# Optimization experiments

Measured on AMD Instinct MI355X. Metric: run time of the kernel, lower is better.

The kernel has to match this reference:

```python
import jax, jax.numpy as jnp
import numpy as np

T, B, N_LABELS = 128, 512, 512
HIDDEN, SEMANTIC = 1024, 1024
THRESHOLD, DECAY = 1.0, 0.95


def setup_inputs() -> dict:
    key = jax.random.key(0)
    k1, k2, k3 = jax.random.split(key, 3)
    spike_seq = (jax.random.uniform(k1, (T, B, N_LABELS)) < 0.1).astype(jnp.float32)
    W1 = jax.random.normal(k2, (HIDDEN, N_LABELS), dtype=jnp.float32) * 0.05
    W2 = jax.random.normal(k3, (SEMANTIC, HIDDEN), dtype=jnp.float32) * 0.05
    return {"spike_seq": spike_seq, "W1": W1, "W2": W2}


def reference(spike_seq, W1, W2):
    """LIF two-layer SNN. LIF step: v = decay*v + input; spike = (v > threshold);
    hard reset to zero on spike. Returns time-averaged spikes of layer1 and layer2."""
    dtype = spike_seq.dtype
    Bsz = spike_seq.shape[1]

    def lif(v, x):
        v = DECAY * v + x
        spk = (v > THRESHOLD).astype(dtype)
        return spk, v * (1.0 - spk)

    def step(carry, x_t):
        v1, v2 = carry
        spk1, v1 = lif(v1, x_t @ W1.T)          # (B, HIDDEN)
        spk2, v2 = lif(v2, spk1 @ W2.T)         # (B, SEMANTIC)
        return (v1, v2), (spk1, spk2)

    v1_0 = jnp.zeros((Bsz, W1.shape[0]), dtype)
    v2_0 = jnp.zeros((Bsz, W2.shape[0]), dtype)
    _, (spk1_all, spk2_all) = jax.lax.scan(step, (v1_0, v2_0), spike_seq)
    return spk1_all.mean(axis=0), spk2_all.mean(axis=0)
```

## Files before the change

kernel.cpp:

```cpp
#include <hip/hip_runtime.h>


#define T_STEPS 128
#define BATCH   512
#define NLAB    512
#define HID     1024
#define SEM     1024

__global__ __launch_bounds__(256) void transpose32(const float* __restrict__ in,
                                                   float* __restrict__ out,
                                                   int R, int C) {
    __shared__ float tile[32][33];
    const int c0 = blockIdx.x * 32, r0 = blockIdx.y * 32;
    const int x = threadIdx.x, y0 = threadIdx.y;
#pragma unroll
    for (int i = 0; i < 32; i += 8)
        tile[y0 + i][x] = in[(size_t)(r0 + y0 + i) * C + (c0 + x)];
    __syncthreads();
#pragma unroll
    for (int i = 0; i < 32; i += 8)
        out[(size_t)(c0 + y0 + i) * R + (r0 + x)] = tile[x][y0 + i];
}

__device__ __forceinline__ void gather4(const int* __restrict__ list,
                                        int lo, int hi,
                                        const float* __restrict__ base,
                                        float s[4]) {
    float s0 = 0.0f, s1 = 0.0f, s2 = 0.0f, s3 = 0.0f;
    int k = lo;
    for (; k + 16 <= hi; k += 16) {
        float4 wv[16];
#pragma unroll
        for (int j = 0; j < 16; ++j) {
            const int row = __builtin_amdgcn_readfirstlane(list[k + j]);
            wv[j] = *reinterpret_cast<const float4*>(base + ((size_t)row << 10));
        }
#pragma unroll
        for (int j = 0; j < 16; ++j) {
            s0 = __fadd_rn(s0, wv[j].x);
            s1 = __fadd_rn(s1, wv[j].y);
            s2 = __fadd_rn(s2, wv[j].z);
            s3 = __fadd_rn(s3, wv[j].w);
        }
    }
    for (; k + 8 <= hi; k += 8) {
        float4 wv[8];
#pragma unroll
        for (int j = 0; j < 8; ++j) {
            const int row = __builtin_amdgcn_readfirstlane(list[k + j]);
            wv[j] = *reinterpret_cast<const float4*>(base + ((size_t)row << 10));
        }
#pragma unroll
        for (int j = 0; j < 8; ++j) {
            s0 = __fadd_rn(s0, wv[j].x);
            s1 = __fadd_rn(s1, wv[j].y);
            s2 = __fadd_rn(s2, wv[j].z);
            s3 = __fadd_rn(s3, wv[j].w);
        }
    }
    for (; k < hi; ++k) {
        const int row = __builtin_amdgcn_readfirstlane(list[k]);
        const float4 wv = *reinterpret_cast<const float4*>(base + ((size_t)row << 10));
        s0 = __fadd_rn(s0, wv.x);
        s1 = __fadd_rn(s1, wv.y);
        s2 = __fadd_rn(s2, wv.z);
        s3 = __fadd_rn(s3, wv.w);
    }
    s[0] = s0; s[1] = s1; s[2] = s2; s[3] = s3;
}

__global__ __launch_bounds__(256)
void snn_kernel(const float* __restrict__ spikes,
                const float* __restrict__ w1t,
                const float* __restrict__ w2t,
                float* __restrict__ out) {
    __shared__ int wc1[4];
    __shared__ int wc1p;
    __shared__ int wc2[4];
    __shared__ int wc2p[3];
    __shared__ __align__(16) int list1[NLAB];
    __shared__ __align__(16) int list2[HID];

    const int b    = blockIdx.x;
    const int tid  = threadIdx.x;
    const int w    = tid >> 6;
    const int lane = tid & 63;
    const unsigned long long below = (1ull << lane) - 1ull;

    float v1[4] = {0.0f, 0.0f, 0.0f, 0.0f};
    float v2[4] = {0.0f, 0.0f, 0.0f, 0.0f};
    int   c1[4] = {0, 0, 0, 0};
    int   c2[4] = {0, 0, 0, 0};

    const float* sp_b = spikes + (size_t)b * NLAB + 2 * tid;
    const float* w1b  = w1t + 4 * tid;
    const float* w2b  = w2t + 4 * tid;

    float2 sv = *reinterpret_cast<const float2*>(sp_b);

    for (int t = 0; t < T_STEPS; ++t) {
        const bool a0 = (sv.x != 0.0f);
        const bool a1 = (sv.y != 0.0f);
        const unsigned long long m0 = __ballot(a0);
        const unsigned long long m1 = __ballot(a1);
        if (lane == 0) {
            wc1[w] = __popcll(m0) + __popcll(m1);
            if (w == 2)
                wc1p = __popcll(m0 & 0xFFFFFFFFull) + __popcll(m1 & 0xFFFFFFFFull);
        }
        const int pre1 = __popcll(m0 & below) + __popcll(m1 & below);
        __syncthreads();

        {
            int base = 0;
            for (int i = 0; i < w; ++i) base += wc1[i];
            int p = base + pre1;
            if (a0) list1[p++] = 2 * tid;
            if (a1) list1[p]   = 2 * tid + 1;
        }
        __syncthreads();

        if (t + 1 < T_STEPS)
            sv = *reinterpret_cast<const float2*>(sp_b + (size_t)(t + 1) * (BATCH * NLAB));

        bool spk0, spk1, spk2, spk3;
        int  preh;
        {
            const int nA = wc1[0] + wc1[1] + wc1p;
            const int n1 = wc1[0] + wc1[1] + wc1[2] + wc1[3];
            float xA[4], xB[4];
            gather4(list1, 0,  nA, w1b, xA);
            gather4(list1, nA, n1, w1b, xB);
#pragma unroll
            for (int j = 0; j < 4; ++j) {
                const float x1 = __fadd_rn(xA[j], xB[j]);
                v1[j] = __fadd_rn(__fmul_rn(0.95f, v1[j]), x1);
            }
            spk0 = (v1[0] > 1.0f); if (spk0) { c1[0]++; v1[0] = 0.0f; }
            spk1 = (v1[1] > 1.0f); if (spk1) { c1[1]++; v1[1] = 0.0f; }
            spk2 = (v1[2] > 1.0f); if (spk2) { c1[2]++; v1[2] = 0.0f; }
            spk3 = (v1[3] > 1.0f); if (spk3) { c1[3]++; v1[3] = 0.0f; }

            const unsigned long long b0 = __ballot(spk0);
            const unsigned long long b1 = __ballot(spk1);
            const unsigned long long b2 = __ballot(spk2);
            const unsigned long long b3 = __ballot(spk3);
            if (lane == 0) {
                wc2[w] = __popcll(b0) + __popcll(b1) + __popcll(b2) + __popcll(b3);
                if (w == 1)
                    wc2p[0] = __popcll(b0 & 0xFFFFull) + __popcll(b1 & 0xFFFFull)
                            + __popcll(b2 & 0xFFFFull) + __popcll(b3 & 0xFFFFull);
                if (w == 2)
                    wc2p[1] = __popcll(b0 & 0xFFFFFFFFull) + __popcll(b1 & 0xFFFFFFFFull)
                            + __popcll(b2 & 0xFFFFFFFFull) + __popcll(b3 & 0xFFFFFFFFull);
                if (w == 3)
                    wc2p[2] = __popcll(b0 & 0xFFFFFFFFFFFFull) + __popcll(b1 & 0xFFFFFFFFFFFFull)
                            + __popcll(b2 & 0xFFFFFFFFFFFFull) + __popcll(b3 & 0xFFFFFFFFFFFFull);
            }
            preh = __popcll(b0 & below) + __popcll(b1 & below)
                 + __popcll(b2 & below) + __popcll(b3 & below);
        }
        __syncthreads();

        {
            int base = 0;
            for (int i = 0; i < w; ++i) base += wc2[i];
            int p = base + preh;
            if (spk0) list2[p++] = 4 * tid;
            if (spk1) list2[p++] = 4 * tid + 1;
            if (spk2) list2[p++] = 4 * tid + 2;
            if (spk3) list2[p]   = 4 * tid + 3;
        }
        __syncthreads();

        {
            const int nA = wc2[0] + wc2p[0];
            const int nB = wc2[0] + wc2[1] + wc2p[1];
            const int nC = wc2[0] + wc2[1] + wc2[2] + wc2p[2];
            const int n2 = wc2[0] + wc2[1] + wc2[2] + wc2[3];
            float t1[4], t2[4], t3[4], t4[4];
            gather4(list2, 0,  nA, w2b, t1);
            gather4(list2, nA, nB, w2b, t2);
            gather4(list2, nB, nC, w2b, t3);
            gather4(list2, nC, n2, w2b, t4);
#pragma unroll
            for (int j = 0; j < 4; ++j) {
                const float x2 = __fadd_rn(__fadd_rn(__fadd_rn(t1[j], t2[j]), t3[j]), t4[j]);
                v2[j] = __fadd_rn(__fmul_rn(0.95f, v2[j]), x2);
                if (v2[j] > 1.0f) { c2[j]++; v2[j] = 0.0f; }
            }
        }
        __syncthreads();
    }

    const float sc = 1.0f / 128.0f;
    const float4 o1 = make_float4((float)c1[0] * sc, (float)c1[1] * sc,
                                  (float)c1[2] * sc, (float)c1[3] * sc);
    *reinterpret_cast<float4*>(out + (size_t)b * HID + 4 * tid) = o1;
    const float4 o2 = make_float4((float)c2[0] * sc, (float)c2[1] * sc,
                                  (float)c2[2] * sc, (float)c2[3] * sc);
    *reinterpret_cast<float4*>(out + (size_t)BATCH * HID + (size_t)b * SEM + 4 * tid) = o2;
}

extern "C" void kernel_launch(void* const* d_in, const int* in_sizes, int n_in,
                              void* d_out, int out_size, void* d_ws, size_t ws_size,
                              hipStream_t stream) {
    const float* spikes = (const float*)d_in[0];
    const float* W1     = (const float*)d_in[1];
    const float* W2     = (const float*)d_in[2];
    float* out = (float*)d_out;

    float* w1t = (float*)d_ws;
    float* w2t = w1t + (size_t)NLAB * HID;

    dim3 tb(32, 8);
    transpose32<<<dim3(NLAB / 32, HID / 32), tb, 0, stream>>>(W1, w1t, HID, NLAB);
    transpose32<<<dim3(HID / 32, SEM / 32),  tb, 0, stream>>>(W2, w2t, SEM, HID);

    snn_kernel<<<BATCH, 256, 0, stream>>>(spikes, w1t, w2t, out);
}
```

Before: 1.563 ms.

## Process two batch rows per block sharing union spike lists and weight loads

Each block now handles two batch rows. It builds one union list of active inputs and hidden spikes, with per-row mask bits packed into each entry, so each gathered weight row is loaded once and applied to both rows through masked packed FMAs. This cuts weight gather traffic per row and halves the grid to 256 blocks, which may underfill the GPU's CUs. The union lists are longer than either row's own list, and the masked FMA arithmetic (adding 0*w instead of skipping) could differ slightly from the original sequential adds.

```diff
diff --git a/kernel.cpp b/kernel.cpp
--- a/kernel.cpp
+++ b/kernel.cpp
@@ -6,6 +6,8 @@
 #define NLAB    512
 #define HID     1024
 #define SEM     1024
+
+typedef float f32x2 __attribute__((ext_vector_type(2)));
 
 __global__ __launch_bounds__(256) void transpose32(const float* __restrict__ in,
                                                    float* __restrict__ out,
@@ -22,51 +24,66 @@
         out[(size_t)(c0 + y0 + i) * R + (r0 + x)] = tile[x][y0 + i];
 }
 
-__device__ __forceinline__ void gather4(const int* __restrict__ list,
+__device__ __forceinline__ void gatherU(const int* __restrict__ list,
                                         int lo, int hi,
                                         const float* __restrict__ base,
-                                        float s[4]) {
-    float s0 = 0.0f, s1 = 0.0f, s2 = 0.0f, s3 = 0.0f;
+                                        f32x2 s[4]) {
+    f32x2 s00 = {0.0f, 0.0f}, s01 = {0.0f, 0.0f};
+    f32x2 s10 = {0.0f, 0.0f}, s11 = {0.0f, 0.0f};
     int k = lo;
     for (; k + 16 <= hi; k += 16) {
+        int    e[16];
         float4 wv[16];
 #pragma unroll
         for (int j = 0; j < 16; ++j) {
-            const int row = __builtin_amdgcn_readfirstlane(list[k + j]);
-            wv[j] = *reinterpret_cast<const float4*>(base + ((size_t)row << 10));
+            e[j] = __builtin_amdgcn_readfirstlane(list[k + j]);
+            wv[j] = *reinterpret_cast<const float4*>(base + ((size_t)(e[j] & 0xFFFF) << 10));
         }
 #pragma unroll
         for (int j = 0; j < 16; ++j) {
-            s0 = __fadd_rn(s0, wv[j].x);
-            s1 = __fadd_rn(s1, wv[j].y);
-            s2 = __fadd_rn(s2, wv[j].z);
-            s3 = __fadd_rn(s3, wv[j].w);
+            const float f0 = (e[j] & 0x10000) ? 1.0f : 0.0f;
+            const float f1 = (e[j] & 0x20000) ? 1.0f : 0.0f;
+            const f32x2 m0 = {f0, f0}, m1 = {f1, f1};
+            const f32x2 w01 = {wv[j].x, wv[j].y}, w23 = {wv[j].z, wv[j].w};
+            s00 = __builtin_elementwise_fma(m0, w01, s00);
+            s01 = __builtin_elementwise_fma(m0, w23, s01);
+            s10 = __builtin_elementwise_fma(m1, w01, s10);
+            s11 = __builtin_elementwise_fma(m1, w23, s11);
         }
     }
     for (; k + 8 <= hi; k += 8) {
+        int    e[8];
         float4 wv[8];
 #pragma unroll
         for (int j = 0; j < 8; ++j) {
-            const int row = __builtin_amdgcn_readfirstlane(list[k + j]);
-            wv[j] = *reinterpret_cast<const float4*>(base + ((size_t)row << 10));
+            e[j] = __builtin_amdgcn_readfirstlane(list[k + j]);
+            wv[j] = *reinterpret_cast<const float4*>(base + ((size_t)(e[j] & 0xFFFF) << 10));
         }
 #pragma unroll
         for (int j = 0; j < 8; ++j) {
-            s0 = __fadd_rn(s0, wv[j].x);
-            s1 = __fadd_rn(s1, wv[j].y);
-            s2 = __fadd_rn(s2, wv[j].z);
-            s3 = __fadd_rn(s3, wv[j].w);
+            const float f0 = (e[j] & 0x10000) ? 1.0f : 0.0f;
+            const float f1 = (e[j] & 0x20000) ? 1.0f : 0.0f;
+            const f32x2 m0 = {f0, f0}, m1 = {f1, f1};
+            const f32x2 w01 = {wv[j].x, wv[j].y}, w23 = {wv[j].z, wv[j].w};
+            s00 = __builtin_elementwise_fma(m0, w01, s00);
+            s01 = __builtin_elementwise_fma(m0, w23, s01);
+            s10 = __builtin_elementwise_fma(m1, w01, s10);
+            s11 = __builtin_elementwise_fma(m1, w23, s11);
         }
     }
     for (; k < hi; ++k) {
-        const int row = __builtin_amdgcn_readfirstlane(list[k]);
-        const float4 wv = *reinterpret_cast<const float4*>(base + ((size_t)row << 10));
-        s0 = __fadd_rn(s0, wv.x);
-        s1 = __fadd_rn(s1, wv.y);
-        s2 = __fadd_rn(s2, wv.z);
-        s3 = __fadd_rn(s3, wv.w);
-    }
-    s[0] = s0; s[1] = s1; s[2] = s2; s[3] = s3;
+        const int e = __builtin_amdgcn_readfirstlane(list[k]);
+        const float4 wv = *reinterpret_cast<const float4*>(base + ((size_t)(e & 0xFFFF) << 10));
+        const float f0 = (e & 0x10000) ? 1.0f : 0.0f;
+        const float f1 = (e & 0x20000) ? 1.0f : 0.0f;
+        const f32x2 m0 = {f0, f0}, m1 = {f1, f1};
+        const f32x2 w01 = {wv.x, wv.y}, w23 = {wv.z, wv.w};
+        s00 = __builtin_elementwise_fma(m0, w01, s00);
+        s01 = __builtin_elementwise_fma(m0, w23, s01);
+        s10 = __builtin_elementwise_fma(m1, w01, s10);
+        s11 = __builtin_elementwise_fma(m1, w23, s11);
+    }
+    s[0] = s00; s[1] = s01; s[2] = s10; s[3] = s11;
 }
 
 __global__ __launch_bounds__(256)
@@ -81,28 +98,33 @@
     __shared__ __align__(16) int list1[NLAB];
     __shared__ __align__(16) int list2[HID];
 
-    const int b    = blockIdx.x;
     const int tid  = threadIdx.x;
     const int w    = tid >> 6;
     const int lane = tid & 63;
     const unsigned long long below = (1ull << lane) - 1ull;
 
-    float v1[4] = {0.0f, 0.0f, 0.0f, 0.0f};
-    float v2[4] = {0.0f, 0.0f, 0.0f, 0.0f};
-    int   c1[4] = {0, 0, 0, 0};
-    int   c2[4] = {0, 0, 0, 0};
-
-    const float* sp_b = spikes + (size_t)b * NLAB + 2 * tid;
-    const float* w1b  = w1t + 4 * tid;
-    const float* w2b  = w2t + 4 * tid;
-
-    float2 sv = *reinterpret_cast<const float2*>(sp_b);
+    const int b0 = 2 * blockIdx.x;
+
+    f32x2 v1[4] = {{0,0},{0,0},{0,0},{0,0}};
+    f32x2 v2[4] = {{0,0},{0,0},{0,0},{0,0}};
+    int   c1[8] = {0,0,0,0,0,0,0,0};
+    int   c2[8] = {0,0,0,0,0,0,0,0};
+
+    const float* sp0 = spikes + (size_t)b0 * NLAB + 2 * tid;
+    const float* sp1 = sp0 + NLAB;
+    const float* w1b = w1t + 4 * tid;
+    const float* w2b = w2t + 4 * tid;
+
+    float2 sv0 = *reinterpret_cast<const float2*>(sp0);
+    float2 sv1 = *reinterpret_cast<const float2*>(sp1);
 
     for (int t = 0; t < T_STEPS; ++t) {
-        const bool a0 = (sv.x != 0.0f);
-        const bool a1 = (sv.y != 0.0f);
-        const unsigned long long m0 = __ballot(a0);
-        const unsigned long long m1 = __ballot(a1);
+        const bool a00 = (sv0.x != 0.0f), a01 = (sv0.y != 0.0f);
+        const bool a10 = (sv1.x != 0.0f), a11 = (sv1.y != 0.0f);
+        const bool u0 = a00 | a10;
+        const bool u1 = a01 | a11;
+        const unsigned long long m0 = __ballot(u0);
+        const unsigned long long m1 = __ballot(u1);
         if (lane == 0) {
             wc1[w] = __popcll(m0) + __popcll(m1);
             if (w == 2)
@@ -115,50 +137,60 @@
             int base = 0;
             for (int i = 0; i < w; ++i) base += wc1[i];
             int p = base + pre1;
-            if (a0) list1[p++] = 2 * tid;
-            if (a1) list1[p]   = 2 * tid + 1;
-        }
-        __syncthreads();
-
-        if (t + 1 < T_STEPS)
-            sv = *reinterpret_cast<const float2*>(sp_b + (size_t)(t + 1) * (BATCH * NLAB));
-
-        bool spk0, spk1, spk2, spk3;
+            if (u0) list1[p++] = (2 * tid)     | (a00 ? 0x10000 : 0) | (a10 ? 0x20000 : 0);
+            if (u1) list1[p]   = (2 * tid + 1) | (a01 ? 0x10000 : 0) | (a11 ? 0x20000 : 0);
+        }
+        __syncthreads();
+
+        if (t + 1 < T_STEPS) {
+            sv0 = *reinterpret_cast<const float2*>(sp0 + (size_t)(t + 1) * (BATCH * NLAB));
+            sv1 = *reinterpret_cast<const float2*>(sp1 + (size_t)(t + 1) * (BATCH * NLAB));
+        }
+
+        bool sp00, sp01, sp02, sp03, sp10, sp11, sp12, sp13;
         int  preh;
         {
             const int nA = wc1[0] + wc1[1] + wc1p;
             const int n1 = wc1[0] + wc1[1] + wc1[2] + wc1[3];
-            float xA[4], xB[4];
-            gather4(list1, 0,  nA, w1b, xA);
-            gather4(list1, nA, n1, w1b, xB);
+            f32x2 xA[4], xB[4];
+            gatherU(list1, 0,  nA, w1b, xA);
+            gatherU(list1, nA, n1, w1b, xB);
 #pragma unroll
             for (int j = 0; j < 4; ++j) {
-                const float x1 = __fadd_rn(xA[j], xB[j]);
-                v1[j] = __fadd_rn(__fmul_rn(0.95f, v1[j]), x1);
+                const f32x2 x1 = xA[j] + xB[j];
+                v1[j] = (v1[j] * 0.95f) + x1;
             }
-            spk0 = (v1[0] > 1.0f); if (spk0) { c1[0]++; v1[0] = 0.0f; }
-            spk1 = (v1[1] > 1.0f); if (spk1) { c1[1]++; v1[1] = 0.0f; }
-            spk2 = (v1[2] > 1.0f); if (spk2) { c1[2]++; v1[2] = 0.0f; }
-            spk3 = (v1[3] > 1.0f); if (spk3) { c1[3]++; v1[3] = 0.0f; }
-
-            const unsigned long long b0 = __ballot(spk0);
-            const unsigned long long b1 = __ballot(spk1);
-            const unsigned long long b2 = __ballot(spk2);
-            const unsigned long long b3 = __ballot(spk3);
+            sp00 = (v1[0].x > 1.0f); if (sp00) { c1[0]++; v1[0].x = 0.0f; }
+            sp01 = (v1[0].y > 1.0f); if (sp01) { c1[1]++; v1[0].y = 0.0f; }
+            sp02 = (v1[1].x > 1.0f); if (sp02) { c1[2]++; v1[1].x = 0.0f; }
+            sp03 = (v1[1].y > 1.0f); if (sp03) { c1[3]++; v1[1].y = 0.0f; }
+            sp10 = (v1[2].x > 1.0f); if (sp10) { c1[4]++; v1[2].x = 0.0f; }
+            sp11 = (v1[2].y > 1.0f); if (sp11) { c1[5]++; v1[2].y = 0.0f; }
+            sp12 = (v1[3].x > 1.0f); if (sp12) { c1[6]++; v1[3].x = 0.0f; }
+            sp13 = (v1[3].y > 1.0f); if (sp13) { c1[7]++; v1[3].y = 0.0f; }
+
+            const bool uc0 = sp00 | sp10;
+            const bool uc1 = sp01 | sp11;
+            const bool uc2 = sp02 | sp12;
+            const bool uc3 = sp03 | sp13;
+            const unsigned long long b0m = __ballot(uc0);
+            const unsigned long long b1m = __ballot(uc1);
+            const unsigned long long b2m = __ballot(uc2);
+            const unsigned long long b3m = __ballot(uc3);
             if (lane == 0) {
-                wc2[w] = __popcll(b0) + __popcll(b1) + __popcll(b2) + __popcll(b3);
+                wc2[w] = __popcll(b0m) + __popcll(b1m) + __popcll(b2m) + __popcll(b3m);
                 if (w == 1)
-                    wc2p[0] = __popcll(b0 & 0xFFFFull) + __popcll(b1 & 0xFFFFull)
-                            + __popcll(b2 & 0xFFFFull) + __popcll(b3 & 0xFFFFull);
+                    wc2p[0] = __popcll(b0m & 0xFFFFull) + __popcll(b1m & 0xFFFFull)
+                            + __popcll(b2m & 0xFFFFull) + __popcll(b3m & 0xFFFFull);
                 if (w == 2)
-                    wc2p[1] = __popcll(b0 & 0xFFFFFFFFull) + __popcll(b1 & 0xFFFFFFFFull)
-                            + __popcll(b2 & 0xFFFFFFFFull) + __popcll(b3 & 0xFFFFFFFFull);
+                    wc2p[1] = __popcll(b0m & 0xFFFFFFFFull) + __popcll(b1m & 0xFFFFFFFFull)
+                            + __popcll(b2m & 0xFFFFFFFFull) + __popcll(b3m & 0xFFFFFFFFull);
                 if (w == 3)
-                    wc2p[2] = __popcll(b0 & 0xFFFFFFFFFFFFull) + __popcll(b1 & 0xFFFFFFFFFFFFull)
-                            + __popcll(b2 & 0xFFFFFFFFFFFFull) + __popcll(b3 & 0xFFFFFFFFFFFFull);
+                    wc2p[2] = __popcll(b0m & 0xFFFFFFFFFFFFull) + __popcll(b1m & 0xFFFFFFFFFFFFull)
+                            + __popcll(b2m & 0xFFFFFFFFFFFFull) + __popcll(b3m & 0xFFFFFFFFFFFFull);
             }
-            preh = __popcll(b0 & below) + __popcll(b1 & below)
-                 + __popcll(b2 & below) + __popcll(b3 & below);
+            preh = __popcll(b0m & below) + __popcll(b1m & below)
+                 + __popcll(b2m & below) + __popcll(b3m & below);
         }
         __syncthreads();
 
@@ -166,10 +198,10 @@
             int base = 0;
             for (int i = 0; i < w; ++i) base += wc2[i];
             int p = base + preh;
-            if (spk0) list2[p++] = 4 * tid;
-            if (spk1) list2[p++] = 4 * tid + 1;
-            if (spk2) list2[p++] = 4 * tid + 2;
-            if (spk3) list2[p]   = 4 * tid + 3;
+            if (sp00 | sp10) list2[p++] = (4 * tid)     | (sp00 ? 0x10000 : 0) | (sp10 ? 0x20000 : 0);
+            if (sp01 | sp11) list2[p++] = (4 * tid + 1) | (sp01 ? 0x10000 : 0) | (sp11 ? 0x20000 : 0);
+            if (sp02 | sp12) list2[p++] = (4 * tid + 2) | (sp02 ? 0x10000 : 0) | (sp12 ? 0x20000 : 0);
+            if (sp03 | sp13) list2[p]   = (4 * tid + 3) | (sp03 ? 0x10000 : 0) | (sp13 ? 0x20000 : 0);
         }
         __syncthreads();
 
@@ -178,28 +210,46 @@
             const int nB = wc2[0] + wc2[1] + wc2p[1];
             const int nC = wc2[0] + wc2[1] + wc2[2] + wc2p[2];
             const int n2 = wc2[0] + wc2[1] + wc2[2] + wc2[3];
-            float t1[4], t2[4], t3[4], t4[4];
-            gather4(list2, 0,  nA, w2b, t1);
-            gather4(list2, nA, nB, w2b, t2);
-            gather4(list2, nB, nC, w2b, t3);
-            gather4(list2, nC, n2, w2b, t4);
+            f32x2 t1[4], t2[4], t3[4], t4[4];
+            gatherU(list2, 0,  nA, w2b, t1);
+            gatherU(list2, nA, nB, w2b, t2);
+            gatherU(list2, nB, nC, w2b, t3);
+            gatherU(list2, nC, n2, w2b, t4);
 #pragma unroll
             for (int j = 0; j < 4; ++j) {
-                const float x2 = __fadd_rn(__fadd_rn(__fadd_rn(t1[j], t2[j]), t3[j]), t4[j]);
-                v2[j] = __fadd_rn(__fmul_rn(0.95f, v2[j]), x2);
-                if (v2[j] > 1.0f) { c2[j]++; v2[j] = 0.0f; }
+                const f32x2 x2 = ((t1[j] + t2[j]) + t3[j]) + t4[j];
+                v2[j] = (v2[j] * 0.95f) + x2;
             }
+            if (v2[0].x > 1.0f) { c2[0]++; v2[0].x = 0.0f; }
+            if (v2[0].y > 1.0f) { c2[1]++; v2[0].y = 0.0f; }
+            if (v2[1].x > 1.0f) { c2[2]++; v2[1].x = 0.0f; }
+            if (v2[1].y > 1.0f) { c2[3]++; v2[1].y = 0.0f; }
+            if (v2[2].x > 1.0f) { c2[4]++; v2[2].x = 0.0f; }
+            if (v2[2].y > 1.0f) { c2[5]++; v2[2].y = 0.0f; }
+            if (v2[3].x > 1.0f) { c2[6]++; v2[3].x = 0.0f; }
+            if (v2[3].y > 1.0f) { c2[7]++; v2[3].y = 0.0f; }
         }
         __syncthreads();
     }
 
     const float sc = 1.0f / 128.0f;
-    const float4 o1 = make_float4((float)c1[0] * sc, (float)c1[1] * sc,
-                                  (float)c1[2] * sc, (float)c1[3] * sc);
-    *reinterpret_cast<float4*>(out + (size_t)b * HID + 4 * tid) = o1;
-    const float4 o2 = make_float4((float)c2[0] * sc, (float)c2[1] * sc,
-                                  (float)c2[2] * sc, (float)c2[3] * sc);
-    *reinterpret_cast<float4*>(out + (size_t)BATCH * HID + (size_t)b * SEM + 4 * tid) = o2;
+    {
+        const float4 o = make_float4((float)c1[0] * sc, (float)c1[1] * sc,
+                                     (float)c1[2] * sc, (float)c1[3] * sc);
+        *reinterpret_cast<float4*>(out + (size_t)b0 * HID + 4 * tid) = o;
+        const float4 o2 = make_float4((float)c1[4] * sc, (float)c1[5] * sc,
+                                      (float)c1[6] * sc, (float)c1[7] * sc);
+        *reinterpret_cast<float4*>(out + (size_t)(b0 + 1) * HID + 4 * tid) = o2;
+    }
+    {
+        float* ob = out + (size_t)BATCH * HID;
+        const float4 o = make_float4((float)c2[0] * sc, (float)c2[1] * sc,
+                                     (float)c2[2] * sc, (float)c2[3] * sc);
+        *reinterpret_cast<float4*>(ob + (size_t)b0 * SEM + 4 * tid) = o;
+        const float4 o2 = make_float4((float)c2[4] * sc, (float)c2[5] * sc,
+                                      (float)c2[6] * sc, (float)c2[7] * sc);
+        *reinterpret_cast<float4*>(ob + (size_t)(b0 + 1) * SEM + 4 * tid) = o2;
+    }
 }
 
 extern "C" void kernel_launch(void* const* d_in, const int* in_sizes, int n_in,
@@ -217,5 +267,5 @@
     transpose32<<<dim3(NLAB / 32, HID / 32), tb, 0, stream>>>(W1, w1t, HID, NLAB);
     transpose32<<<dim3(HID / 32, SEM / 32),  tb, 0, stream>>>(W2, w2t, SEM, HID);
 
-    snn_kernel<<<BATCH, 256, 0, stream>>>(spikes, w1t, w2t, out);
-}
+    snn_kernel<<<BATCH / 2, 256, 0, stream>>>(spikes, w1t, w2t, out);
+}
```

New measurement: 1.886 ms. +20.7%, slower.
